# Performance work log

Measured on AMD Instinct MI355X. Metric: run time of the kernel, lower is better.

Reference implementation:

```python
import jax, jax.numpy as jnp
import numpy as np
import math

B, S, IN, D, H = 128, 128, 16, 256, 256


def _gates(pre):
    i, f, g, o = jnp.split(pre, 4, axis=-1)
    return jax.nn.sigmoid(i), jax.nn.sigmoid(f), jnp.tanh(g), jax.nn.sigmoid(o)


def _lstm_dir(xp, Whh):
    # xp: [B,S,4H] precomputed input projection (+ both biases); scan over time.
    b = xp.shape[0]
    h_dim = Whh.shape[1]

    def step(carry, xt):
        h, c = carry
        i, f, g, o = _gates(xt + h @ Whh.T)
        c = f * c + i * g
        h = o * jnp.tanh(c)
        return (h, c), h

    init = (jnp.zeros((b, h_dim), xp.dtype), jnp.zeros((b, h_dim), xp.dtype))
    (hT, cT), hs = jax.lax.scan(step, init, jnp.swapaxes(xp, 0, 1))
    return jnp.swapaxes(hs, 0, 1), hT, cT


def _layernorm(x, g, b, eps=1e-5):
    m = jnp.mean(x, -1, keepdims=True)
    v = jnp.mean((x - m) ** 2, -1, keepdims=True)
    return (x - m) * jax.lax.rsqrt(v + eps) * g + b


def _forward(x, proj_W, proj_b, ln_g, ln_b,
             Wih_f, Whh_f, bih_f, bhh_f,
             Wih_b, Whh_b, bih_b, bhh_b,
             Wih_d, Whh_d, bih_d, bhh_d,
             hb_W, hb_b, cb_W, cb_b,
             gW1, gW2, gv, pW1, pW2, pv):
    b, s, _ = x.shape
    h_dim = Whh_d.shape[1]
    # Projector: Linear -> Tanh -> LayerNorm
    emb = _layernorm(jnp.tanh(x @ proj_W.T + proj_b), ln_g, ln_b)  # [B,S,D]
    # Bidirectional LSTM encoder (PyTorch gate order i,f,g,o)
    hf, hTf, cTf = _lstm_dir(emb @ Wih_f.T + (bih_f + bhh_f), Whh_f)
    hb_rev, hTb, cTb = _lstm_dir((emb @ Wih_b.T + (bih_b + bhh_b))[:, ::-1], Whh_b)
    hb_out = hb_rev[:, ::-1]
    enc = jnp.concatenate([hf, hb_out], -1)  # [B,S,2H]
    # Bridges to decoder init state
    h = jnp.tanh(jnp.concatenate([hTf, hTb], -1) @ hb_W.T + hb_b)
    c = jnp.tanh(jnp.concatenate([cTf, cTb], -1) @ cb_W.T + cb_b)
    dec_in = jnp.mean(enc, axis=1)  # [B,2H]
    # W1(encoder_outputs) is step-invariant: precompute once for both attentions
    g_ref = enc @ gW1.T  # [B,S,H]
    p_ref = enc @ pW1.T  # [B,S,H]
    scale = 1.0 / math.sqrt(h_dim)
    mask0 = jnp.zeros((b, s), jnp.bool_)

    def step(carry, _):
        h, c, mask, dec_in = carry
        # LSTMCell
        i, f, g, o = _gates(dec_in @ Wih_d.T + h @ Whh_d.T + bih_d + bhh_d)
        c = f * c + i * g
        h = o * jnp.tanh(c)
        # glimpse attention
        gs = jnp.tanh(g_ref + (h @ gW2.T)[:, None, :]) @ gv * scale  # [B,S]
        gp = jax.nn.softmax(jnp.where(mask, -1e9, gs), axis=1)
        ctx = jnp.einsum('bs,bsh->bh', gp, enc)  # [B,2H]
        # pointer attention (query = h + context[:, :H])
        ps = jnp.tanh(p_ref + ((h + ctx[:, :h_dim]) @ pW2.T)[:, None, :]) @ pv * scale
        ps = jnp.where(mask, -1e9, ps)  # masked scores are the returned logits
        sel = jnp.argmax(ps, axis=1)  # argmax(softmax(ps)) == argmax(ps)
        mask = mask | jax.nn.one_hot(sel, s, dtype=jnp.bool_)
        dec_in = jnp.take_along_axis(enc, sel[:, None, None], axis=1)[:, 0]
        return (h, c, mask, dec_in), (ps, sel)

    _, (logits, ptrs) = jax.lax.scan(step, (h, c, mask0, dec_in), None, length=s)
    return jnp.swapaxes(logits, 0, 1), jnp.swapaxes(ptrs, 0, 1)


def setup_inputs() -> dict:
    key = jax.random.key(0)
    ks = iter(jax.random.split(key, 20))

    def w(*shape):
        return jax.random.normal(next(ks), shape, jnp.float32) * 0.05

    z = lambda *shape: jnp.zeros(shape, jnp.float32)
    return {
        'x': jax.random.normal(next(ks), (B, S, IN), jnp.float32),
        'proj_W': w(D, IN), 'proj_b': z(D), 'ln_g': jnp.ones((D,), jnp.float32), 'ln_b': z(D),
        'Wih_f': w(4 * H, D), 'Whh_f': w(4 * H, H), 'bih_f': z(4 * H), 'bhh_f': z(4 * H),
        'Wih_b': w(4 * H, D), 'Whh_b': w(4 * H, H), 'bih_b': z(4 * H), 'bhh_b': z(4 * H),
        'Wih_d': w(4 * H, 2 * H), 'Whh_d': w(4 * H, H), 'bih_d': z(4 * H), 'bhh_d': z(4 * H),
        'hb_W': w(H, 2 * H), 'hb_b': z(H), 'cb_W': w(H, 2 * H), 'cb_b': z(H),
        'gW1': w(H, 2 * H), 'gW2': w(H, H), 'gv': w(H),
        'pW1': w(H, 2 * H), 'pW2': w(H, H), 'pv': w(H),
    }


def reference(x, proj_W, proj_b, ln_g, ln_b, Wih_f, Whh_f, bih_f, bhh_f, Wih_b, Whh_b, bih_b, bhh_b, Wih_d, Whh_d, bih_d, bhh_d, hb_W, hb_b, cb_W, cb_b, gW1, gW2, gv, pW1, pW2, pv):
    return _forward(x, proj_W, proj_b, ln_g, ln_b, Wih_f, Whh_f, bih_f, bhh_f, Wih_b, Whh_b, bih_b, bhh_b, Wih_d, Whh_d, bih_d, bhh_d, hb_W, hb_b, cb_W, cb_b, gW1, gW2, gv, pW1, pW2, pv)
```

## Files before the change

### kernel.cpp

```cpp
#include <hip/hip_runtime.h>
#include <cstdint>
#include <cstddef>

#define DEVINL __device__ __forceinline__

typedef float f32x4 __attribute__((ext_vector_type(4)));

DEVINL float ntload1(const float* p) {
    return __builtin_nontemporal_load(p);
}
DEVINL f32x4 ld4(const float* p) {
    return *reinterpret_cast<const f32x4*>(p);
}

DEVINL float frcp(float x) { return __builtin_amdgcn_rcpf(x); }
DEVINL float ftanh_fast(float x) {
    float e = __expf(2.0f * x);
    return 1.0f - 2.0f * frcp(e + 1.0f);
}
DEVINL float sig_precise(float x) { return 1.0f / (1.0f + expf(-x)); }
DEVINL float tanh_precise(float x) { return tanhf(x); }

#define BB 128
#define SS 128
#define IND 16
#define DD 256
#define HH 256
#define H4 1024
#define H2 512

__global__ __launch_bounds__(256) void k_proj_ln(
    const float* __restrict__ x, const float* __restrict__ projW,
    const float* __restrict__ projB, const float* __restrict__ ln_g,
    const float* __restrict__ ln_b, float* __restrict__ emb)
{
    __shared__ float Wl[256 * 17];
    __shared__ float xl[16];
    __shared__ float red[256];
    const int row = blockIdx.x;
    const int tid = threadIdx.x;
    for (int idx = tid; idx < 256 * 16; idx += 256) {
        int d = idx >> 4, i = idx & 15;
        Wl[d * 17 + i] = projW[idx];
    }
    if (tid < 16) xl[tid] = x[row * 16 + tid];
    __syncthreads();
    float acc = projB[tid];
#pragma unroll
    for (int i = 0; i < 16; ++i) acc = fmaf(Wl[tid * 17 + i], xl[i], acc);
    float v = tanh_precise(acc);
    red[tid] = v;
    __syncthreads();
    for (int s2 = 128; s2 > 0; s2 >>= 1) { if (tid < s2) red[tid] += red[tid + s2]; __syncthreads(); }
    float mean = red[0] * (1.0f / 256.0f);
    __syncthreads();
    float dlt = v - mean;
    red[tid] = dlt * dlt;
    __syncthreads();
    for (int s2 = 128; s2 > 0; s2 >>= 1) { if (tid < s2) red[tid] += red[tid + s2]; __syncthreads(); }
    float var = red[0] * (1.0f / 256.0f);
    float rs = 1.0f / sqrtf(var + 1e-5f);
    emb[(size_t)row * 256 + tid] = dlt * rs * ln_g[tid] + ln_b[tid];
}

__global__ __launch_bounds__(256) void k_gemm_nt(
    const float* __restrict__ A, int lda,
    const float* __restrict__ Bm,
    float* __restrict__ C,
    int M, int N, int K,
    const float* __restrict__ bias1, const float* __restrict__ bias2,
    int flags)
{
    __shared__ __align__(16) float As[16][132];
    __shared__ __align__(16) float Bs[16][132];
    const int tid = threadIdx.x;
    const int m0 = blockIdx.x * 128;
    const int n0 = blockIdx.y * 128;
    const int r = tid >> 1, half = tid & 1;
    const int tm = tid & 15, tn = tid >> 4;
    float acc[8][8];
#pragma unroll
    for (int i = 0; i < 8; ++i)
#pragma unroll
        for (int j = 0; j < 8; ++j) acc[i][j] = 0.0f;

    for (int k0 = 0; k0 < K; k0 += 16) {
        const float4* pa = reinterpret_cast<const float4*>(&A[(size_t)(m0 + r) * lda + k0 + half * 8]);
        float4 a0 = pa[0], a1 = pa[1];
        const float4* pb = reinterpret_cast<const float4*>(&Bm[(size_t)(n0 + r) * K + k0 + half * 8]);
        float4 b0 = pb[0], b1 = pb[1];
        __syncthreads();
        const int kb = half * 8;
        As[kb + 0][r] = a0.x; As[kb + 1][r] = a0.y; As[kb + 2][r] = a0.z; As[kb + 3][r] = a0.w;
        As[kb + 4][r] = a1.x; As[kb + 5][r] = a1.y; As[kb + 6][r] = a1.z; As[kb + 7][r] = a1.w;
        Bs[kb + 0][r] = b0.x; Bs[kb + 1][r] = b0.y; Bs[kb + 2][r] = b0.z; Bs[kb + 3][r] = b0.w;
        Bs[kb + 4][r] = b1.x; Bs[kb + 5][r] = b1.y; Bs[kb + 6][r] = b1.z; Bs[kb + 7][r] = b1.w;
        __syncthreads();
#pragma unroll
        for (int kk = 0; kk < 16; ++kk) {
            const float4 xa0 = *reinterpret_cast<const float4*>(&As[kk][tm * 8]);
            const float4 xa1 = *reinterpret_cast<const float4*>(&As[kk][tm * 8 + 4]);
            const float4 xb0 = *reinterpret_cast<const float4*>(&Bs[kk][tn * 8]);
            const float4 xb1 = *reinterpret_cast<const float4*>(&Bs[kk][tn * 8 + 4]);
            const float av[8] = {xa0.x, xa0.y, xa0.z, xa0.w, xa1.x, xa1.y, xa1.z, xa1.w};
            const float bv[8] = {xb0.x, xb0.y, xb0.z, xb0.w, xb1.x, xb1.y, xb1.z, xb1.w};
#pragma unroll
            for (int i = 0; i < 8; ++i)
#pragma unroll
                for (int j = 0; j < 8; ++j) acc[i][j] = fmaf(av[i], bv[j], acc[i][j]);
        }
    }
    const int nb = n0 + tn * 8;
    float bias[8];
#pragma unroll
    for (int j = 0; j < 8; ++j) {
        float bbv = 0.0f;
        if (bias1) bbv += bias1[nb + j];
        if (bias2) bbv += bias2[nb + j];
        bias[j] = bbv;
    }
#pragma unroll
    for (int i = 0; i < 8; ++i) {
        const size_t m = (size_t)(m0 + tm * 8 + i);
        float o[8];
#pragma unroll
        for (int j = 0; j < 8; ++j) {
            float vv = acc[i][j] + bias[j];
            if (flags & 1) vv = tanh_precise(vv);
            o[j] = vv;
        }
        float4* pc = reinterpret_cast<float4*>(&C[m * N + nb]);
        pc[0] = make_float4(o[0], o[1], o[2], o[3]);
        pc[1] = make_float4(o[4], o[5], o[6], o[7]);
    }
}

__global__ __launch_bounds__(512, 2) void k_lstm(
    const float* __restrict__ Whh_f, const float* __restrict__ Whh_b,
    const float* __restrict__ xf, const float* __restrict__ xb,
    float* __restrict__ enc, float* __restrict__ hT, float* __restrict__ cT)
{
    const int wg = blockIdx.x;
    const int dir = wg >> 7;
    const int bat = wg & 127;
    const float* W = dir ? Whh_b : Whh_f;
    const float* xin = dir ? xb : xf;
    const int tid = threadIdx.x;
    const int oct = tid & 7, jg = tid >> 3;

    __shared__ __align__(16) float h_lds[256];
    __shared__ float pre_lds[1024];

    if (tid < 256) h_lds[tid] = 0.0f;
    float c_reg = 0.0f;
    __syncthreads();

    for (int t = 0; t < SS; ++t) {
        const int st = dir ? (SS - 1 - t) : t;
        float hreg[32];
#pragma unroll
        for (int i = 0; i < 8; ++i) {
            f32x4 v = ld4(&h_lds[i * 32 + oct * 4]);
            hreg[i * 4 + 0] = v.x; hreg[i * 4 + 1] = v.y;
            hreg[i * 4 + 2] = v.z; hreg[i * 4 + 3] = v.w;
        }
        {
            f32x4 wA[8], wB[8];
            {
                const float* bp = &W[(size_t)jg * 256 + oct * 4];
#pragma unroll
                for (int i = 0; i < 8; ++i) wA[i] = ld4(bp + i * 32);
            }
            auto wstep = [&](f32x4 (&cur)[8], f32x4 (&nxt)[8], int q) {
                if (q < 15) {
                    const float* bp = &W[(size_t)((q + 1) * 64 + jg) * 256 + oct * 4];
#pragma unroll
                    for (int i = 0; i < 8; ++i) nxt[i] = ld4(bp + i * 32);
                }
                float a0 = 0.0f;
#pragma unroll
                for (int i = 0; i < 8; ++i) {
                    a0 = fmaf(cur[i].x, hreg[i * 4 + 0], a0);
                    a0 = fmaf(cur[i].y, hreg[i * 4 + 1], a0);
                    a0 = fmaf(cur[i].z, hreg[i * 4 + 2], a0);
                    a0 = fmaf(cur[i].w, hreg[i * 4 + 3], a0);
                }
                a0 += __shfl_xor(a0, 1); a0 += __shfl_xor(a0, 2); a0 += __shfl_xor(a0, 4);
                if (oct == 0) pre_lds[q * 64 + jg] = a0;
            };
#pragma unroll 1
            for (int q = 0; q < 16; q += 2) { wstep(wA, wB, q); wstep(wB, wA, q + 1); }
        }
        __syncthreads();
        if (tid < 256) {
            const int gc = tid;
            const float* xrow = &xin[((size_t)bat * SS + st) * 1024];
            float pi = pre_lds[gc]       + ntload1(&xrow[gc]);
            float pf = pre_lds[256 + gc] + ntload1(&xrow[256 + gc]);
            float pg = pre_lds[512 + gc] + ntload1(&xrow[512 + gc]);
            float po = pre_lds[768 + gc] + ntload1(&xrow[768 + gc]);
            float ig = sig_precise(pi), fg = sig_precise(pf);
            float gg = tanh_precise(pg), og = sig_precise(po);
            float cn = fmaf(fg, c_reg, ig * gg);
            float hn = og * tanh_precise(cn);
            c_reg = cn;
            h_lds[gc] = hn;
            enc[((size_t)bat * SS + st) * 512 + dir * 256 + gc] = hn;
            if (t == SS - 1) {
                hT[(size_t)bat * 512 + dir * 256 + gc] = hn;
                cT[(size_t)bat * 512 + dir * 256 + gc] = cn;
            }
        }
        __syncthreads();
    }
}

__global__ __launch_bounds__(256) void k_meanw(const float* __restrict__ encW, float* __restrict__ pre0)
{
    const int b = blockIdx.x;
    const int tid = threadIdx.x;
    const float4* base = reinterpret_cast<const float4*>(&encW[(size_t)b * SS * 1024]);
    float sx = 0.0f, sy = 0.0f, sz = 0.0f, sw = 0.0f;
    for (int s = 0; s < SS; ++s) {
        float4 v = base[s * 256 + tid];
        sx += v.x; sy += v.y; sz += v.z; sw += v.w;
    }
    float4* out = reinterpret_cast<float4*>(&pre0[(size_t)b * 1024]);
    out[tid] = make_float4(sx * (1.0f / 128.0f), sy * (1.0f / 128.0f), sz * (1.0f / 128.0f), sw * (1.0f / 128.0f));
}

__global__ __launch_bounds__(1024) void k_decoder(
    const float* __restrict__ Whh_d,
    const float* __restrict__ gW2, const float* __restrict__ pW2,
    const float* __restrict__ gv, const float* __restrict__ pv,
    const float* __restrict__ g_ref, const float* __restrict__ p_ref,
    const float* __restrict__ encP, const float* __restrict__ encW,
    const float* __restrict__ pre0, const float* __restrict__ h0,
    const float* __restrict__ c0,
    float* __restrict__ out_logits, float* __restrict__ out_ptrs)
{
    const int b = blockIdx.x;
    const int tid = threadIdx.x;
    const int oct = tid & 7;
    const int jg128 = tid >> 3;
    const int wid = tid >> 6, lane = tid & 63;
    const int ajg = (tid & 511) >> 3;
    const int wjg = (tid & 511) >> 3;

    __shared__ __align__(16) float h_lds[256];
    __shared__ float c_lds[256];
    __shared__ float wacc_lds[1024];
    __shared__ float row_lds[1024];
    __shared__ __align__(16) float hgp[512];
    __shared__ __align__(16) float hp_lds[256];
    __shared__ __align__(16) float gv_lds[256];
    __shared__ __align__(16) float pv_lds[256];
    __shared__ float sc_arr[128];
    __shared__ float e_arr[128];
    __shared__ __align__(16) float hp_half[8][256];
    __shared__ int mask_lds[128];
    __shared__ int ulist[128];
    __shared__ int ucount_s;
    __shared__ float Z_s;
    __shared__ int sel_s;

    if (tid < 256) {
        gv_lds[tid] = gv[tid];
        pv_lds[tid] = pv[tid];
        h_lds[tid] = h0[(size_t)b * 256 + tid];
        c_lds[tid] = c0[(size_t)b * 256 + tid];
    }
    if (tid < 128) mask_lds[tid] = 0;
    if (tid == 0) sel_s = -1;
    const float* grefb = g_ref + (size_t)b * SS * 256;
    const float* prefb = p_ref + (size_t)b * SS * 256;
    const float* encPb = encP + (size_t)b * SS * 256;
    __syncthreads();

    {
        float hreg0[32];
#pragma unroll
        for (int i = 0; i < 8; ++i) {
            f32x4 v = ld4(&h_lds[i * 32 + oct * 4]);
            hreg0[i * 4 + 0] = v.x; hreg0[i * 4 + 1] = v.y;
            hreg0[i * 4 + 2] = v.z; hreg0[i * 4 + 3] = v.w;
        }
        f32x4 wA[8], wB[8];
        {
            const float* bp = &Whh_d[(size_t)jg128 * 256 + oct * 4];
#pragma unroll
            for (int i = 0; i < 8; ++i) wA[i] = ld4(bp + i * 32);
        }
        auto pw = [&](f32x4 (&cur)[8], f32x4 (&nxt)[8], int q) {
            if (q < 7) {
                const float* bp = &Whh_d[(size_t)((q + 1) * 128 + jg128) * 256 + oct * 4];
#pragma unroll
                for (int i = 0; i < 8; ++i) nxt[i] = ld4(bp + i * 32);
            }
            float a0 = 0.0f;
#pragma unroll
            for (int i = 0; i < 8; ++i) {
                a0 = fmaf(cur[i].x, hreg0[i * 4 + 0], a0);
                a0 = fmaf(cur[i].y, hreg0[i * 4 + 1], a0);
                a0 = fmaf(cur[i].z, hreg0[i * 4 + 2], a0);
                a0 = fmaf(cur[i].w, hreg0[i * 4 + 3], a0);
            }
            a0 += __shfl_xor(a0, 1); a0 += __shfl_xor(a0, 2); a0 += __shfl_xor(a0, 4);
            if (oct == 0) wacc_lds[q * 128 + jg128] = a0;
        };
#pragma unroll 1
        for (int q = 0; q < 8; q += 2) { pw(wA, wB, q); pw(wB, wA, q + 1); }
    }
    __syncthreads();

    for (int t = 0; t < SS; ++t) {
        {
            const int sel = sel_s;
            const float* src = (sel < 0) ? &pre0[(size_t)b * 1024]
                                         : &encW[((size_t)(b * SS + sel)) * 1024];
            row_lds[tid] = src[tid];
        }
        if (tid >= 128 && tid < 256) sc_arr[tid - 128] = -1e9f;
        if (tid < 64) {
            const unsigned long long lowmask = (1ull << lane) - 1ull;
            const bool u0 = (mask_lds[lane] == 0);
            const unsigned long long b0m = __ballot(u0);
            if (u0) ulist[__popcll(b0m & lowmask)] = lane;
            const bool u1 = (mask_lds[lane + 64] == 0);
            const unsigned long long b1m = __ballot(u1);
            const int c0 = __popcll(b0m);
            if (u1) ulist[c0 + __popcll(b1m & lowmask)] = lane + 64;
            if (lane == 0) ucount_s = c0 + __popcll(b1m);
        }
        __syncthreads();
        if (tid < 256) {
            const int ch = tid;
            float pi = wacc_lds[ch]       + row_lds[ch];
            float pf = wacc_lds[256 + ch] + row_lds[256 + ch];
            float pg = wacc_lds[512 + ch] + row_lds[512 + ch];
            float po = wacc_lds[768 + ch] + row_lds[768 + ch];
            float ig = sig_precise(pi), fg = sig_precise(pf);
            float gg = tanh_precise(pg), og = sig_precise(po);
            float cn = fmaf(fg, c_lds[ch], ig * gg);
            float hn = og * tanh_precise(cn);
            c_lds[ch] = cn;
            h_lds[ch] = hn;
        }
        __syncthreads();
        float hreg[32];
#pragma unroll
        for (int i = 0; i < 8; ++i) {
            f32x4 v = ld4(&h_lds[i * 32 + oct * 4]);
            hreg[i * 4 + 0] = v.x; hreg[i * 4 + 1] = v.y;
            hreg[i * 4 + 2] = v.z; hreg[i * 4 + 3] = v.w;
        }
        auto wround = [&](int q) {
            const float* bp = &Whh_d[(size_t)(q * 64 + wjg) * 256 + oct * 4];
            f32x4 w[8];
#pragma unroll
            for (int i = 0; i < 8; ++i) w[i] = ld4(bp + i * 32);
            float a0 = 0.0f;
#pragma unroll
            for (int i = 0; i < 8; ++i) {
                a0 = fmaf(w[i].x, hreg[i * 4 + 0], a0);
                a0 = fmaf(w[i].y, hreg[i * 4 + 1], a0);
                a0 = fmaf(w[i].z, hreg[i * 4 + 2], a0);
                a0 = fmaf(w[i].w, hreg[i * 4 + 3], a0);
            }
            a0 += __shfl_xor(a0, 1); a0 += __shfl_xor(a0, 2); a0 += __shfl_xor(a0, 4);
            if (oct == 0) wacc_lds[q * 64 + wjg] = a0;
        };
        if (tid < 512) {
            f32x4 wA[8], wB[8];
            {
                const float* src0 = (ajg < 256) ? &gW2[(size_t)ajg * 256] : &pW2[(size_t)(ajg - 256) * 256];
#pragma unroll
                for (int i = 0; i < 8; ++i) wA[i] = ld4(src0 + oct * 4 + i * 32);
            }
            auto p3 = [&](f32x4 (&cur)[8], f32x4 (&nxt)[8], int q) {
                if (q < 7) {
                    const int r2 = (q + 1) * 64 + ajg;
                    const float* src = (r2 < 256) ? &gW2[(size_t)r2 * 256] : &pW2[(size_t)(r2 - 256) * 256];
#pragma unroll
                    for (int i = 0; i < 8; ++i) nxt[i] = ld4(src + oct * 4 + i * 32);
                }
                float a0 = 0.0f;
#pragma unroll
                for (int i = 0; i < 8; ++i) {
                    a0 = fmaf(cur[i].x, hreg[i * 4 + 0], a0);
                    a0 = fmaf(cur[i].y, hreg[i * 4 + 1], a0);
                    a0 = fmaf(cur[i].z, hreg[i * 4 + 2], a0);
                    a0 = fmaf(cur[i].w, hreg[i * 4 + 3], a0);
                }
                a0 += __shfl_xor(a0, 1); a0 += __shfl_xor(a0, 2); a0 += __shfl_xor(a0, 4);
                if (oct == 0) hgp[q * 64 + ajg] = a0;
            };
#pragma unroll 1
            for (int q = 0; q < 8; q += 2) { p3(wA, wB, q); p3(wB, wA, q + 1); }
        } else {
            wround(0); wround(1); wround(2);
        }
        __syncthreads();
        if (tid < 512) {
            const int uc = ucount_s;
#pragma unroll 1
            for (int rep = 0; rep < 2; ++rep) {
                const int k = ajg + rep * 64;
                if (k < uc) {
                    const int r = ulist[k];
                    const float* gr = &grefb[(size_t)r * 256 + oct * 4];
                    f32x4 g0[8];
#pragma unroll
                    for (int i = 0; i < 8; ++i) g0[i] = ld4(gr + i * 32);
                    float part = 0.0f;
#pragma unroll
                    for (int i = 0; i < 8; ++i) {
                        const int d = i * 32 + oct * 4;
                        const f32x4 hh = ld4(&hgp[d]);
                        const f32x4 vv = ld4(&gv_lds[d]);
                        part = fmaf(ftanh_fast(g0[i].x + hh.x), vv.x, part);
                        part = fmaf(ftanh_fast(g0[i].y + hh.y), vv.y, part);
                        part = fmaf(ftanh_fast(g0[i].z + hh.z), vv.z, part);
                        part = fmaf(ftanh_fast(g0[i].w + hh.w), vv.w, part);
                    }
                    part += __shfl_xor(part, 1); part += __shfl_xor(part, 2); part += __shfl_xor(part, 4);
                    if (oct == 0) sc_arr[r] = part * 0.0625f;
                }
            }
        } else {
            wround(3); wround(4); wround(5);
        }
        __syncthreads();
        if (tid < 64) {
            float s0 = sc_arr[lane], s1 = sc_arr[lane + 64];
            float m = fmaxf(s0, s1);
#pragma unroll
            for (int mk = 1; mk < 64; mk <<= 1) m = fmaxf(m, __shfl_xor(m, mk));
            float e0 = expf(s0 - m), e1 = expf(s1 - m);
            e_arr[lane] = e0; e_arr[lane + 64] = e1;
            float z = e0 + e1;
#pragma unroll
            for (int mk = 1; mk < 64; mk <<= 1) z += __shfl_xor(z, mk);
            if (lane == 0) Z_s = z;
        } else if (tid >= 512) {
            wround(6); wround(7);
        }
        __syncthreads();
        if (tid < 512) {
            const int uc = ucount_s;
            const int d4 = lane * 4;
            float ax = 0.0f, ay = 0.0f, az = 0.0f, aw = 0.0f;
            if (wid * 16 < uc) {
#pragma unroll 1
                for (int half = 0; half < 2; ++half) {
                    const int k0 = wid * 16 + half * 8;
                    if (k0 < uc) {
                        f32x4 p0[8]; float ee[8];
#pragma unroll
                        for (int i = 0; i < 8; ++i) {
                            const int k = k0 + i;
                            const int kc = (k < uc) ? k : (uc - 1);
                            const int s = ulist[kc];
                            ee[i] = (k < uc) ? e_arr[s] : 0.0f;
                            p0[i] = ld4(&encPb[(size_t)s * 256 + d4]);
                        }
#pragma unroll
                        for (int i = 0; i < 8; ++i) {
                            ax = fmaf(p0[i].x, ee[i], ax); ay = fmaf(p0[i].y, ee[i], ay);
                            az = fmaf(p0[i].z, ee[i], az); aw = fmaf(p0[i].w, ee[i], aw);
                        }
                    }
                }
            }
            *reinterpret_cast<float4*>(&hp_half[wid][d4]) = make_float4(ax, ay, az, aw);
        } else {
            wround(8); wround(9); wround(10);
        }
        __syncthreads();
        if (tid < 256) {
            float s = 0.0f;
#pragma unroll
            for (int k = 0; k < 8; ++k) s += hp_half[k][tid];
            hp_lds[tid] = hgp[256 + tid] + s * frcp(Z_s);
        } else if (tid >= 512) {
            wround(11); wround(12);
        }
        __syncthreads();
        if (tid < 512) {
            const int uc = ucount_s;
#pragma unroll 1
            for (int rep = 0; rep < 2; ++rep) {
                const int k = ajg + rep * 64;
                if (k < uc) {
                    const int r = ulist[k];
                    const float* pr = &prefb[(size_t)r * 256 + oct * 4];
                    f32x4 g0[8];
#pragma unroll
                    for (int i = 0; i < 8; ++i) g0[i] = ld4(pr + i * 32);
                    float part = 0.0f;
#pragma unroll
                    for (int i = 0; i < 8; ++i) {
                        const int d = i * 32 + oct * 4;
                        const f32x4 hh = ld4(&hp_lds[d]);
                        const f32x4 vv = ld4(&pv_lds[d]);
                        part = fmaf(ftanh_fast(g0[i].x + hh.x), vv.x, part);
                        part = fmaf(ftanh_fast(g0[i].y + hh.y), vv.y, part);
                        part = fmaf(ftanh_fast(g0[i].z + hh.z), vv.z, part);
                        part = fmaf(ftanh_fast(g0[i].w + hh.w), vv.w, part);
                    }
                    part += __shfl_xor(part, 1); part += __shfl_xor(part, 2); part += __shfl_xor(part, 4);
                    if (oct == 0) sc_arr[r] = part * 0.0625f;
                }
            }
        } else {
            wround(13); wround(14); wround(15);
        }
        __syncthreads();
        if (tid < 128) {
            out_logits[((size_t)(b * SS + t)) * SS + tid] = sc_arr[tid];
        }
        if (tid < 64) {
            float v = sc_arr[lane];
            int idx = lane;
            float v2 = sc_arr[lane + 64];
            if (v2 > v) { v = v2; idx = lane + 64; }
#pragma unroll
            for (int mk = 1; mk < 64; mk <<= 1) {
                float ov = __shfl_xor(v, mk);
                int oi = __shfl_xor(idx, mk);
                if (ov > v || (ov == v && oi < idx)) { v = ov; idx = oi; }
            }
            if (lane == 0) {
                sel_s = idx;
                mask_lds[idx] = 1;
                out_ptrs[(size_t)b * SS + t] = (float)idx;
            }
        }
        __syncthreads();
    }
}

extern "C" void kernel_launch(void* const* d_in, const int* in_sizes, int n_in,
                              void* d_out, int out_size, void* d_ws, size_t ws_size,
                              hipStream_t stream)
{
    (void)in_sizes; (void)n_in; (void)out_size; (void)ws_size;
    const float* x      = (const float*)d_in[0];
    const float* proj_W = (const float*)d_in[1];
    const float* proj_b = (const float*)d_in[2];
    const float* ln_g   = (const float*)d_in[3];
    const float* ln_b   = (const float*)d_in[4];
    const float* Wih_f  = (const float*)d_in[5];
    const float* Whh_f  = (const float*)d_in[6];
    const float* bih_f  = (const float*)d_in[7];
    const float* bhh_f  = (const float*)d_in[8];
    const float* Wih_b  = (const float*)d_in[9];
    const float* Whh_b  = (const float*)d_in[10];
    const float* bih_b  = (const float*)d_in[11];
    const float* bhh_b  = (const float*)d_in[12];
    const float* Wih_d  = (const float*)d_in[13];
    const float* Whh_d  = (const float*)d_in[14];
    const float* bih_d  = (const float*)d_in[15];
    const float* bhh_d  = (const float*)d_in[16];
    const float* hb_W   = (const float*)d_in[17];
    const float* hb_b   = (const float*)d_in[18];
    const float* cb_W   = (const float*)d_in[19];
    const float* cb_b   = (const float*)d_in[20];
    const float* gW1    = (const float*)d_in[21];
    const float* gW2    = (const float*)d_in[22];
    const float* gv     = (const float*)d_in[23];
    const float* pW1    = (const float*)d_in[24];
    const float* pW2    = (const float*)d_in[25];
    const float* pv     = (const float*)d_in[26];

    float* ws = (float*)d_ws;
    const size_t o_hT    = 0;
    const size_t o_cT    = 65536;
    const size_t o_h0    = 131072;
    const size_t o_c0    = 163840;
    const size_t o_pre0  = 196608;
    const size_t o_emb   = 0;
    const size_t o_xf    = 4194304;
    const size_t o_xb    = o_xf + 16777216;
    const size_t o_enc   = o_xb + 16777216;
    const size_t o_encW  = o_xf;
    const size_t o_gref  = o_xb;
    const size_t o_pref  = o_xb + 4194304;
    const size_t o_encP  = o_xb + 8388608;

    float* emb  = ws + o_emb;
    float* xf   = ws + o_xf;
    float* xb   = ws + o_xb;
    float* enc  = ws + o_enc;
    float* hT   = ws + o_hT;
    float* cT   = ws + o_cT;
    float* h0b  = ws + o_h0;
    float* c0b  = ws + o_c0;
    float* pre0 = ws + o_pre0;
    float* encW = ws + o_encW;
    float* gref = ws + o_gref;
    float* pref = ws + o_pref;
    float* encP = ws + o_encP;

    float* out_logits = (float*)d_out;
    float* out_ptrs   = out_logits + (size_t)BB * SS * SS;

    k_proj_ln<<<BB * SS, 256, 0, stream>>>(x, proj_W, proj_b, ln_g, ln_b, emb);
    {
        dim3 g(128, 8);
        k_gemm_nt<<<g, 256, 0, stream>>>(emb, 256, Wih_f, xf, 16384, 1024, 256, bih_f, bhh_f, 0);
        k_gemm_nt<<<g, 256, 0, stream>>>(emb, 256, Wih_b, xb, 16384, 1024, 256, bih_b, bhh_b, 0);
    }
    k_lstm<<<256, 512, 0, stream>>>(Whh_f, Whh_b, xf, xb, enc, hT, cT);
    {
        dim3 g(1, 2);
        k_gemm_nt<<<g, 256, 0, stream>>>(hT, 512, hb_W, h0b, 128, 256, 512, hb_b, nullptr, 1);
        k_gemm_nt<<<g, 256, 0, stream>>>(cT, 512, cb_W, c0b, 128, 256, 512, cb_b, nullptr, 1);
    }
    {
        dim3 g2(128, 2);
        k_gemm_nt<<<g2, 256, 0, stream>>>(enc, 512, gW1, gref, 16384, 256, 512, nullptr, nullptr, 0);
        k_gemm_nt<<<g2, 256, 0, stream>>>(enc, 512, pW1, pref, 16384, 256, 512, nullptr, nullptr, 0);
        dim3 g1(128, 8);
        k_gemm_nt<<<g1, 256, 0, stream>>>(enc, 512, Wih_d, encW, 16384, 1024, 512, bih_d, bhh_d, 0);
        k_gemm_nt<<<g2, 256, 0, stream>>>(enc, 512, pW2, encP, 16384, 256, 256, nullptr, nullptr, 0);
    }
    k_meanw<<<BB, 256, 0, stream>>>(encW, pre0);
    k_decoder<<<128, 1024, 0, stream>>>(Whh_d, gW2, pW2, gv, pv, gref, pref, encP, encW,
                                        pre0, h0b, c0b, out_logits, out_ptrs);
}
```

Baseline: 5.231 ms.

## Merge decoder step phases to cut barriers per timestep

Restructures the per-timestep decoder loop so the LSTM cell update reads its input row directly from global memory and runs alongside score init and mask compaction, removing one barrier. Softmax is computed redundantly by every wave of the attention group, which removes the separate softmax phase and the e_arr buffer. The hp reduction is folded into the pointer-score phase, and the Whh recurrent rounds are redistributed across the remaining phases. Both candidate rows are loaded up front to expose more memory parallelism, at the cost of more registers and redundant exp evaluations.

```diff
diff --git a/kernel.cpp b/kernel.cpp
--- a/kernel.cpp
+++ b/kernel.cpp
@@ -245,18 +245,14 @@
     const int jg128 = tid >> 3;
     const int wid = tid >> 6, lane = tid & 63;
     const int ajg = (tid & 511) >> 3;
-    const int wjg = (tid & 511) >> 3;
 
     __shared__ __align__(16) float h_lds[256];
     __shared__ float c_lds[256];
     __shared__ float wacc_lds[1024];
-    __shared__ float row_lds[1024];
     __shared__ __align__(16) float hgp[512];
-    __shared__ __align__(16) float hp_lds[256];
     __shared__ __align__(16) float gv_lds[256];
     __shared__ __align__(16) float pv_lds[256];
     __shared__ float sc_arr[128];
-    __shared__ float e_arr[128];
     __shared__ __align__(16) float hp_half[8][256];
     __shared__ int mask_lds[128];
     __shared__ int ulist[128];
@@ -275,6 +271,8 @@
     const float* grefb = g_ref + (size_t)b * SS * 256;
     const float* prefb = p_ref + (size_t)b * SS * 256;
     const float* encPb = encP + (size_t)b * SS * 256;
+    const float* pre0b = pre0 + (size_t)b * 1024;
+    const float* encWb = encW + (size_t)b * SS * 1024;
     __syncthreads();
 
     {
@@ -314,14 +312,24 @@
     __syncthreads();
 
     for (int t = 0; t < SS; ++t) {
-        {
+        if (tid < 256) {
+            const int ch = tid;
             const int sel = sel_s;
-            const float* src = (sel < 0) ? &pre0[(size_t)b * 1024]
-                                         : &encW[((size_t)(b * SS + sel)) * 1024];
-            row_lds[tid] = src[tid];
-        }
-        if (tid >= 128 && tid < 256) sc_arr[tid - 128] = -1e9f;
-        if (tid < 64) {
+            const float* src = (sel < 0) ? pre0b : &encWb[(size_t)sel * 1024];
+            float r0 = src[ch], r1 = src[256 + ch], r2 = src[512 + ch], r3 = src[768 + ch];
+            float pi = wacc_lds[ch]       + r0;
+            float pf = wacc_lds[256 + ch] + r1;
+            float pg = wacc_lds[512 + ch] + r2;
+            float po = wacc_lds[768 + ch] + r3;
+            float ig = sig_precise(pi), fg = sig_precise(pf);
+            float gg = tanh_precise(pg), og = sig_precise(po);
+            float cn = fmaf(fg, c_lds[ch], ig * gg);
+            float hn = og * tanh_precise(cn);
+            c_lds[ch] = cn;
+            h_lds[ch] = hn;
+        } else if (tid < 384) {
+            sc_arr[tid - 256] = -1e9f;
+        } else if (tid >= 512 && tid < 576) {
             const unsigned long long lowmask = (1ull << lane) - 1ull;
             const bool u0 = (mask_lds[lane] == 0);
             const unsigned long long b0m = __ballot(u0);
@@ -333,20 +341,6 @@
             if (lane == 0) ucount_s = c0 + __popcll(b1m);
         }
         __syncthreads();
-        if (tid < 256) {
-            const int ch = tid;
-            float pi = wacc_lds[ch]       + row_lds[ch];
-            float pf = wacc_lds[256 + ch] + row_lds[256 + ch];
-            float pg = wacc_lds[512 + ch] + row_lds[512 + ch];
-            float po = wacc_lds[768 + ch] + row_lds[768 + ch];
-            float ig = sig_precise(pi), fg = sig_precise(pf);
-            float gg = tanh_precise(pg), og = sig_precise(po);
-            float cn = fmaf(fg, c_lds[ch], ig * gg);
-            float hn = og * tanh_precise(cn);
-            c_lds[ch] = cn;
-            h_lds[ch] = hn;
-        }
-        __syncthreads();
         float hreg[32];
 #pragma unroll
         for (int i = 0; i < 8; ++i) {
@@ -355,7 +349,7 @@
             hreg[i * 4 + 2] = v.z; hreg[i * 4 + 3] = v.w;
         }
         auto wround = [&](int q) {
-            const float* bp = &Whh_d[(size_t)(q * 64 + wjg) * 256 + oct * 4];
+            const float* bp = &Whh_d[(size_t)(q * 64 + ajg) * 256 + oct * 4];
             f32x4 w[8];
 #pragma unroll
             for (int i = 0; i < 8; ++i) w[i] = ld4(bp + i * 32);
@@ -368,7 +362,7 @@
                 a0 = fmaf(w[i].w, hreg[i * 4 + 3], a0);
             }
             a0 += __shfl_xor(a0, 1); a0 += __shfl_xor(a0, 2); a0 += __shfl_xor(a0, 4);
-            if (oct == 0) wacc_lds[q * 64 + wjg] = a0;
+            if (oct == 0) wacc_lds[q * 64 + ajg] = a0;
         };
         if (tid < 512) {
             f32x4 wA[8], wB[8];
@@ -398,55 +392,69 @@
 #pragma unroll 1
             for (int q = 0; q < 8; q += 2) { p3(wA, wB, q); p3(wB, wA, q + 1); }
         } else {
-            wround(0); wround(1); wround(2);
+            wround(0); wround(1); wround(2); wround(3);
         }
         __syncthreads();
         if (tid < 512) {
             const int uc = ucount_s;
-#pragma unroll 1
-            for (int rep = 0; rep < 2; ++rep) {
-                const int k = ajg + rep * 64;
-                if (k < uc) {
-                    const int r = ulist[k];
-                    const float* gr = &grefb[(size_t)r * 256 + oct * 4];
-                    f32x4 g0[8];
-#pragma unroll
-                    for (int i = 0; i < 8; ++i) g0[i] = ld4(gr + i * 32);
-                    float part = 0.0f;
-#pragma unroll
-                    for (int i = 0; i < 8; ++i) {
-                        const int d = i * 32 + oct * 4;
-                        const f32x4 hh = ld4(&hgp[d]);
-                        const f32x4 vv = ld4(&gv_lds[d]);
-                        part = fmaf(ftanh_fast(g0[i].x + hh.x), vv.x, part);
-                        part = fmaf(ftanh_fast(g0[i].y + hh.y), vv.y, part);
-                        part = fmaf(ftanh_fast(g0[i].z + hh.z), vv.z, part);
-                        part = fmaf(ftanh_fast(g0[i].w + hh.w), vv.w, part);
-                    }
-                    part += __shfl_xor(part, 1); part += __shfl_xor(part, 2); part += __shfl_xor(part, 4);
-                    if (oct == 0) sc_arr[r] = part * 0.0625f;
-                }
+            const bool v0 = (ajg < uc), v1 = (ajg + 64 < uc);
+            const int r0 = v0 ? ulist[ajg] : 0;
+            const int r1 = v1 ? ulist[ajg + 64] : 0;
+            f32x4 gA[8], gB[8];
+            if (v0) {
+                const float* gr = &grefb[(size_t)r0 * 256 + oct * 4];
+#pragma unroll
+                for (int i = 0; i < 8; ++i) gA[i] = ld4(gr + i * 32);
+            }
+            if (v1) {
+                const float* gr = &grefb[(size_t)r1 * 256 + oct * 4];
+#pragma unroll
+                for (int i = 0; i < 8; ++i) gB[i] = ld4(gr + i * 32);
+            }
+            if (v0) {
+                float part = 0.0f;
+#pragma unroll
+                for (int i = 0; i < 8; ++i) {
+                    const int d = i * 32 + oct * 4;
+                    const f32x4 hh = ld4(&hgp[d]);
+                    const f32x4 vv = ld4(&gv_lds[d]);
+                    part = fmaf(ftanh_fast(gA[i].x + hh.x), vv.x, part);
+                    part = fmaf(ftanh_fast(gA[i].y + hh.y), vv.y, part);
+                    part = fmaf(ftanh_fast(gA[i].z + hh.z), vv.z, part);
+                    part = fmaf(ftanh_fast(gA[i].w + hh.w), vv.w, part);
+                }
+                part += __shfl_xor(part, 1); part += __shfl_xor(part, 2); part += __shfl_xor(part, 4);
+                if (oct == 0) sc_arr[r0] = part * 0.0625f;
+            }
+            if (v1) {
+                float part = 0.0f;
+#pragma unroll
+                for (int i = 0; i < 8; ++i) {
+                    const int d = i * 32 + oct * 4;
+                    const f32x4 hh = ld4(&hgp[d]);
+                    const f32x4 vv = ld4(&gv_lds[d]);
+                    part = fmaf(ftanh_fast(gB[i].x + hh.x), vv.x, part);
+                    part = fmaf(ftanh_fast(gB[i].y + hh.y), vv.y, part);
+                    part = fmaf(ftanh_fast(gB[i].z + hh.z), vv.z, part);
+                    part = fmaf(ftanh_fast(gB[i].w + hh.w), vv.w, part);
+                }
+                part += __shfl_xor(part, 1); part += __shfl_xor(part, 2); part += __shfl_xor(part, 4);
+                if (oct == 0) sc_arr[r1] = part * 0.0625f;
             }
         } else {
-            wround(3); wround(4); wround(5);
-        }
-        __syncthreads();
-        if (tid < 64) {
+            wround(4); wround(5); wround(6);
+        }
+        __syncthreads();
+        if (tid < 512) {
             float s0 = sc_arr[lane], s1 = sc_arr[lane + 64];
             float m = fmaxf(s0, s1);
 #pragma unroll
             for (int mk = 1; mk < 64; mk <<= 1) m = fmaxf(m, __shfl_xor(m, mk));
             float e0 = expf(s0 - m), e1 = expf(s1 - m);
-            e_arr[lane] = e0; e_arr[lane + 64] = e1;
             float z = e0 + e1;
 #pragma unroll
             for (int mk = 1; mk < 64; mk <<= 1) z += __shfl_xor(z, mk);
-            if (lane == 0) Z_s = z;
-        } else if (tid >= 512) {
-            wround(6); wround(7);
-        }
-        __syncthreads();
-        if (tid < 512) {
+            if (tid == 0) Z_s = z;
             const int uc = ucount_s;
             const int d4 = lane * 4;
             float ax = 0.0f, ay = 0.0f, az = 0.0f, aw = 0.0f;
@@ -461,7 +469,7 @@
                             const int k = k0 + i;
                             const int kc = (k < uc) ? k : (uc - 1);
                             const int s = ulist[kc];
-                            ee[i] = (k < uc) ? e_arr[s] : 0.0f;
+                            ee[i] = (k < uc) ? expf(sc_arr[s] - m) : 0.0f;
                             p0[i] = ld4(&encPb[(size_t)s * 256 + d4]);
                         }
 #pragma unroll
@@ -474,46 +482,72 @@
             }
             *reinterpret_cast<float4*>(&hp_half[wid][d4]) = make_float4(ax, ay, az, aw);
         } else {
-            wround(8); wround(9); wround(10);
-        }
-        __syncthreads();
-        if (tid < 256) {
-            float s = 0.0f;
-#pragma unroll
-            for (int k = 0; k < 8; ++k) s += hp_half[k][tid];
-            hp_lds[tid] = hgp[256 + tid] + s * frcp(Z_s);
-        } else if (tid >= 512) {
-            wround(11); wround(12);
+            wround(7); wround(8); wround(9);
         }
         __syncthreads();
         if (tid < 512) {
             const int uc = ucount_s;
-#pragma unroll 1
-            for (int rep = 0; rep < 2; ++rep) {
-                const int k = ajg + rep * 64;
-                if (k < uc) {
-                    const int r = ulist[k];
-                    const float* pr = &prefb[(size_t)r * 256 + oct * 4];
-                    f32x4 g0[8];
-#pragma unroll
-                    for (int i = 0; i < 8; ++i) g0[i] = ld4(pr + i * 32);
-                    float part = 0.0f;
-#pragma unroll
-                    for (int i = 0; i < 8; ++i) {
-                        const int d = i * 32 + oct * 4;
-                        const f32x4 hh = ld4(&hp_lds[d]);
-                        const f32x4 vv = ld4(&pv_lds[d]);
-                        part = fmaf(ftanh_fast(g0[i].x + hh.x), vv.x, part);
-                        part = fmaf(ftanh_fast(g0[i].y + hh.y), vv.y, part);
-                        part = fmaf(ftanh_fast(g0[i].z + hh.z), vv.z, part);
-                        part = fmaf(ftanh_fast(g0[i].w + hh.w), vv.w, part);
-                    }
-                    part += __shfl_xor(part, 1); part += __shfl_xor(part, 2); part += __shfl_xor(part, 4);
-                    if (oct == 0) sc_arr[r] = part * 0.0625f;
-                }
+            const bool v0 = (ajg < uc), v1 = (ajg + 64 < uc);
+            const int r0 = v0 ? ulist[ajg] : 0;
+            const int r1 = v1 ? ulist[ajg + 64] : 0;
+            f32x4 gA[8], gB[8];
+            if (v0) {
+                const float* pr = &prefb[(size_t)r0 * 256 + oct * 4];
+#pragma unroll
+                for (int i = 0; i < 8; ++i) gA[i] = ld4(pr + i * 32);
+            }
+            if (v1) {
+                const float* pr = &prefb[(size_t)r1 * 256 + oct * 4];
+#pragma unroll
+                for (int i = 0; i < 8; ++i) gB[i] = ld4(pr + i * 32);
+            }
+            const float rZ = frcp(Z_s);
+            f32x4 hh[8];
+#pragma unroll
+            for (int i = 0; i < 8; ++i) {
+                const int d = i * 32 + oct * 4;
+                f32x4 sum = ld4(&hp_half[0][d]);
+#pragma unroll
+                for (int k = 1; k < 8; ++k) {
+                    f32x4 p = ld4(&hp_half[k][d]);
+                    sum.x += p.x; sum.y += p.y; sum.z += p.z; sum.w += p.w;
+                }
+                f32x4 base = ld4(&hgp[256 + d]);
+                hh[i].x = base.x + sum.x * rZ;
+                hh[i].y = base.y + sum.y * rZ;
+                hh[i].z = base.z + sum.z * rZ;
+                hh[i].w = base.w + sum.w * rZ;
+            }
+            if (v0) {
+                float part = 0.0f;
+#pragma unroll
+                for (int i = 0; i < 8; ++i) {
+                    const int d = i * 32 + oct * 4;
+                    const f32x4 vv = ld4(&pv_lds[d]);
+                    part = fmaf(ftanh_fast(gA[i].x + hh[i].x), vv.x, part);
+                    part = fmaf(ftanh_fast(gA[i].y + hh[i].y), vv.y, part);
+                    part = fmaf(ftanh_fast(gA[i].z + hh[i].z), vv.z, part);
+                    part = fmaf(ftanh_fast(gA[i].w + hh[i].w), vv.w, part);
+                }
+                part += __shfl_xor(part, 1); part += __shfl_xor(part, 2); part += __shfl_xor(part, 4);
+                if (oct == 0) sc_arr[r0] = part * 0.0625f;
+            }
+            if (v1) {
+                float part = 0.0f;
+#pragma unroll
+                for (int i = 0; i < 8; ++i) {
+                    const int d = i * 32 + oct * 4;
+                    const f32x4 vv = ld4(&pv_lds[d]);
+                    part = fmaf(ftanh_fast(gB[i].x + hh[i].x), vv.x, part);
+                    part = fmaf(ftanh_fast(gB[i].y + hh[i].y), vv.y, part);
+                    part = fmaf(ftanh_fast(gB[i].z + hh[i].z), vv.z, part);
+                    part = fmaf(ftanh_fast(gB[i].w + hh[i].w), vv.w, part);
+                }
+                part += __shfl_xor(part, 1); part += __shfl_xor(part, 2); part += __shfl_xor(part, 4);
+                if (oct == 0) sc_arr[r1] = part * 0.0625f;
             }
         } else {
-            wround(13); wround(14); wround(15);
+            wround(10); wround(11); wround(12);
         }
         __syncthreads();
         if (tid < 128) {
@@ -535,6 +569,8 @@
                 mask_lds[idx] = 1;
                 out_ptrs[(size_t)b * SS + t] = (float)idx;
             }
+        } else if (tid >= 512) {
+            wround(13); wround(14); wround(15);
         }
         __syncthreads();
     }
```

Measured after the change: 7.122 ms. +36.2%, slower.

## Fuse decoder LSTM-cell phase with row load and redundantly compute softmax per wave

Applied to the files above, without the earlier changes.

The decoder loop now reads the gate input row straight from global memory inside the LSTM-cell phase instead of staging it in shared memory, which removes one barrier per step. The softmax max and sum are computed redundantly by every wave of the attention half. Each wave then recomputes exp values on the fly instead of reading a shared e_arr, removing a second barrier. The Whh recurrent matvec rounds are redistributed across the remaining phases. This trades extra exp work and uncoalesced-ish global reads for fewer block-wide syncs per step.

```diff
diff --git a/kernel.cpp b/kernel.cpp
--- a/kernel.cpp
+++ b/kernel.cpp
@@ -245,18 +245,15 @@
     const int jg128 = tid >> 3;
     const int wid = tid >> 6, lane = tid & 63;
     const int ajg = (tid & 511) >> 3;
-    const int wjg = (tid & 511) >> 3;
 
     __shared__ __align__(16) float h_lds[256];
     __shared__ float c_lds[256];
     __shared__ float wacc_lds[1024];
-    __shared__ float row_lds[1024];
     __shared__ __align__(16) float hgp[512];
     __shared__ __align__(16) float hp_lds[256];
     __shared__ __align__(16) float gv_lds[256];
     __shared__ __align__(16) float pv_lds[256];
     __shared__ float sc_arr[128];
-    __shared__ float e_arr[128];
     __shared__ __align__(16) float hp_half[8][256];
     __shared__ int mask_lds[128];
     __shared__ int ulist[128];
@@ -275,6 +272,8 @@
     const float* grefb = g_ref + (size_t)b * SS * 256;
     const float* prefb = p_ref + (size_t)b * SS * 256;
     const float* encPb = encP + (size_t)b * SS * 256;
+    const float* pre0b = pre0 + (size_t)b * 1024;
+    const float* encWb = encW + (size_t)b * SS * 1024;
     __syncthreads();
 
     {
@@ -314,14 +313,24 @@
     __syncthreads();
 
     for (int t = 0; t < SS; ++t) {
-        {
+        if (tid < 256) {
+            const int ch = tid;
             const int sel = sel_s;
-            const float* src = (sel < 0) ? &pre0[(size_t)b * 1024]
-                                         : &encW[((size_t)(b * SS + sel)) * 1024];
-            row_lds[tid] = src[tid];
-        }
-        if (tid >= 128 && tid < 256) sc_arr[tid - 128] = -1e9f;
-        if (tid < 64) {
+            const float* src = (sel < 0) ? pre0b : &encWb[(size_t)sel * 1024];
+            float r0 = src[ch], r1 = src[256 + ch], r2 = src[512 + ch], r3 = src[768 + ch];
+            float pi = wacc_lds[ch]       + r0;
+            float pf = wacc_lds[256 + ch] + r1;
+            float pg = wacc_lds[512 + ch] + r2;
+            float po = wacc_lds[768 + ch] + r3;
+            float ig = sig_precise(pi), fg = sig_precise(pf);
+            float gg = tanh_precise(pg), og = sig_precise(po);
+            float cn = fmaf(fg, c_lds[ch], ig * gg);
+            float hn = og * tanh_precise(cn);
+            c_lds[ch] = cn;
+            h_lds[ch] = hn;
+        } else if (tid < 384) {
+            sc_arr[tid - 256] = -1e9f;
+        } else if (tid >= 512 && tid < 576) {
             const unsigned long long lowmask = (1ull << lane) - 1ull;
             const bool u0 = (mask_lds[lane] == 0);
             const unsigned long long b0m = __ballot(u0);
@@ -333,20 +342,6 @@
             if (lane == 0) ucount_s = c0 + __popcll(b1m);
         }
         __syncthreads();
-        if (tid < 256) {
-            const int ch = tid;
-            float pi = wacc_lds[ch]       + row_lds[ch];
-            float pf = wacc_lds[256 + ch] + row_lds[256 + ch];
-            float pg = wacc_lds[512 + ch] + row_lds[512 + ch];
-            float po = wacc_lds[768 + ch] + row_lds[768 + ch];
-            float ig = sig_precise(pi), fg = sig_precise(pf);
-            float gg = tanh_precise(pg), og = sig_precise(po);
-            float cn = fmaf(fg, c_lds[ch], ig * gg);
-            float hn = og * tanh_precise(cn);
-            c_lds[ch] = cn;
-            h_lds[ch] = hn;
-        }
-        __syncthreads();
         float hreg[32];
 #pragma unroll
         for (int i = 0; i < 8; ++i) {
@@ -355,7 +350,7 @@
             hreg[i * 4 + 2] = v.z; hreg[i * 4 + 3] = v.w;
         }
         auto wround = [&](int q) {
-            const float* bp = &Whh_d[(size_t)(q * 64 + wjg) * 256 + oct * 4];
+            const float* bp = &Whh_d[(size_t)(q * 64 + ajg) * 256 + oct * 4];
             f32x4 w[8];
 #pragma unroll
             for (int i = 0; i < 8; ++i) w[i] = ld4(bp + i * 32);
@@ -368,7 +363,7 @@
                 a0 = fmaf(w[i].w, hreg[i * 4 + 3], a0);
             }
             a0 += __shfl_xor(a0, 1); a0 += __shfl_xor(a0, 2); a0 += __shfl_xor(a0, 4);
-            if (oct == 0) wacc_lds[q * 64 + wjg] = a0;
+            if (oct == 0) wacc_lds[q * 64 + ajg] = a0;
         };
         if (tid < 512) {
             f32x4 wA[8], wB[8];
@@ -398,7 +393,7 @@
 #pragma unroll 1
             for (int q = 0; q < 8; q += 2) { p3(wA, wB, q); p3(wB, wA, q + 1); }
         } else {
-            wround(0); wround(1); wround(2);
+            wround(0); wround(1); wround(2); wround(3);
         }
         __syncthreads();
         if (tid < 512) {
@@ -428,25 +423,19 @@
                 }
             }
         } else {
-            wround(3); wround(4); wround(5);
-        }
-        __syncthreads();
-        if (tid < 64) {
+            wround(4); wround(5); wround(6);
+        }
+        __syncthreads();
+        if (tid < 512) {
             float s0 = sc_arr[lane], s1 = sc_arr[lane + 64];
             float m = fmaxf(s0, s1);
 #pragma unroll
             for (int mk = 1; mk < 64; mk <<= 1) m = fmaxf(m, __shfl_xor(m, mk));
             float e0 = expf(s0 - m), e1 = expf(s1 - m);
-            e_arr[lane] = e0; e_arr[lane + 64] = e1;
             float z = e0 + e1;
 #pragma unroll
             for (int mk = 1; mk < 64; mk <<= 1) z += __shfl_xor(z, mk);
-            if (lane == 0) Z_s = z;
-        } else if (tid >= 512) {
-            wround(6); wround(7);
-        }
-        __syncthreads();
-        if (tid < 512) {
+            if (tid == 0) Z_s = z;
             const int uc = ucount_s;
             const int d4 = lane * 4;
             float ax = 0.0f, ay = 0.0f, az = 0.0f, aw = 0.0f;
@@ -461,7 +450,7 @@
                             const int k = k0 + i;
                             const int kc = (k < uc) ? k : (uc - 1);
                             const int s = ulist[kc];
-                            ee[i] = (k < uc) ? e_arr[s] : 0.0f;
+                            ee[i] = (k < uc) ? expf(sc_arr[s] - m) : 0.0f;
                             p0[i] = ld4(&encPb[(size_t)s * 256 + d4]);
                         }
 #pragma unroll
@@ -474,7 +463,7 @@
             }
             *reinterpret_cast<float4*>(&hp_half[wid][d4]) = make_float4(ax, ay, az, aw);
         } else {
-            wround(8); wround(9); wround(10);
+            wround(7); wround(8); wround(9);
         }
         __syncthreads();
         if (tid < 256) {
@@ -483,7 +472,7 @@
             for (int k = 0; k < 8; ++k) s += hp_half[k][tid];
             hp_lds[tid] = hgp[256 + tid] + s * frcp(Z_s);
         } else if (tid >= 512) {
-            wround(11); wround(12);
+            wround(10); wround(11); wround(12);
         }
         __syncthreads();
         if (tid < 512) {
```

After: 5.115 ms (median of 2 runs). 2.2% less time.
